# Kernel optimization log

Hardware: AMD Instinct MI355X
Metric: run time of the kernel (lower is better)

The kernel has to match this reference:

```python
import jax, jax.numpy as jnp
import numpy as np

NBITS = 8
QMAX = 2 ** (NBITS - 1) - 1  # 127
EPS_S = 1e-8


def ste_round(x):
    # straight-through estimator round (matches HAWQ ste_round)
    return x + jax.lax.stop_gradient(jnp.round(x) - x)


def quant_act(x):
    # symmetric per-tensor 8-bit fake quantization (QuantAct)
    s = jnp.maximum(jnp.max(jnp.abs(x)) / QMAX, EPS_S)
    xq = jnp.clip(ste_round(x / s), -QMAX - 1, QMAX)
    return xq * s, s


def quant_weight_per_channel(w, axis=0):
    # symmetric per-output-channel 8-bit fake quantization (weights)
    red = tuple(i for i in range(w.ndim) if i != axis)
    s = jnp.maximum(jnp.max(jnp.abs(w), axis=red, keepdims=True) / QMAX, EPS_S)
    wq = jnp.clip(ste_round(w / s), -QMAX - 1, QMAX)
    return wq * s, s


def setup_inputs() -> dict:
    key = jax.random.key(0)
    ks = jax.random.split(key, 6)
    B, Cin, Cout, H, W = 32, 256, 128, 56, 56
    x = jax.random.normal(ks[0], (B, Cin, H, W), jnp.float32)
    bn_gamma = 1.0 + 0.1 * jax.random.normal(ks[1], (Cin,), jnp.float32)
    bn_beta = 0.1 * jax.random.normal(ks[2], (Cin,), jnp.float32)
    bn_mean = 0.1 * jax.random.normal(ks[3], (Cin,), jnp.float32)
    bn_var = jax.random.uniform(ks[4], (Cin,), jnp.float32, minval=0.5, maxval=1.5)
    conv_w = jax.random.normal(ks[5], (Cout, Cin), jnp.float32) * (1.0 / np.sqrt(Cin))
    return {"x": x, "bn_gamma": bn_gamma, "bn_beta": bn_beta,
            "bn_mean": bn_mean, "bn_var": bn_var, "conv_w": conv_w}


def reference(x, bn_gamma, bn_beta, bn_mean, bn_var, conv_w):
    bn_eps = 1e-5
    # --- QuantAct on incoming activations ---
    x, act_s = quant_act(x)
    # --- QuantBn: fold BN into per-channel scale/shift, quantize folded weight ---
    w_fold = bn_gamma * jax.lax.rsqrt(bn_var + bn_eps)        # [Cin]
    b_fold = bn_beta - bn_mean * w_fold                       # [Cin]
    wq, bn_s = quant_weight_per_channel(w_fold, axis=0)
    x = x * wq[None, :, None, None] + b_fold[None, :, None, None]
    # --- QuantAct1: requantize post-BN output (act_s * bn_s threaded) ---
    x, act_s = quant_act(x)
    # --- ReLU ---
    x = jax.nn.relu(x)
    # --- QuantConv2d: 1x1 conv, per-output-channel quantized weight ---
    cwq, conv_s = quant_weight_per_channel(conv_w, axis=0)    # [Cout, Cin]
    x = jnp.einsum('bchw,oc->bohw', x, cwq)                   # [B, Cout, H, W]
    # --- QuantAct2: requantize post-conv output ---
    x, act_s = quant_act(x)
    # --- QuantAveragePool2d(2,2): pool in integer domain, rescale back ---
    B, C, H, W = x.shape
    x_int = x / act_s
    pooled = x_int.reshape(B, C, H // 2, 2, W // 2, 2).mean(axis=(3, 5))
    x = pooled * act_s
    # --- QuantAct3 ---
    x, act_s = quant_act(x)
    return x, act_s
```

## Files before the change

kernel.cpp:

```cpp
#include <hip/hip_runtime.h>
#include <math.h>

#define QMAXF 127.0f
#define EPSF  1e-8f
#define CIN   256
#define COUT  128
#define HW    3136
#define W_    56
#define NPOOL 3211264
#define POOL_BLOCKS 1792

typedef unsigned short u16;
typedef unsigned int   u32;
typedef __attribute__((ext_vector_type(8))) short s16x8;
typedef __attribute__((ext_vector_type(4))) float f32x4;

#define WQ_OFF   8
#define BF_OFF   264
#define EMAX_OFF 520
#define EMIN_OFF 776
#define CS_OFF   1032
#define CSS2_OFF 1160
#define CWB_OFF  1288
#define LUT_OFF  17672
#define Y_OFF    50440

__device__ __forceinline__ float qclip(float v) {
    return fminf(fmaxf(v, -128.0f), 127.0f);
}
__device__ __forceinline__ u16 bf16bits(float f) {
    return (u16)(__float_as_uint(f) >> 16);
}
__device__ __forceinline__ u32 encf(float f) {
    u32 u = __float_as_uint(f);
    return (u & 0x80000000u) ? ~u : (u | 0x80000000u);
}
__device__ __forceinline__ float decf(u32 k) {
    return __uint_as_float((k & 0x80000000u) ? (k ^ 0x80000000u) : ~k);
}

__device__ __forceinline__ void block_max_atomic(float v, float* red, u32* dst) {
    #pragma unroll
    for (int off = 32; off > 0; off >>= 1) v = fmaxf(v, __shfl_xor(v, off));
    const int lane = threadIdx.x & 63, wid = threadIdx.x >> 6;
    if (lane == 0) red[wid] = v;
    __syncthreads();
    if (threadIdx.x == 0) {
        const int nw = blockDim.x >> 6;
        float m = red[0];
        for (int i = 1; i < nw; ++i) m = fmaxf(m, red[i]);
        atomicMax(dst, __float_as_uint(m));
    }
}

__global__ void k0w(const float* __restrict__ cw, float* __restrict__ ws) {
    const int t = threadIdx.x;
    if (blockIdx.x == COUT) {
        ((u32*)ws)[EMAX_OFF + t] = 0u;
        ((u32*)ws)[EMIN_OFF + t] = 0xFFFFFFFFu;
        if (t < 2) ((u32*)ws)[2 + t] = 0u;
        return;
    }
    __shared__ float red[4];
    const int o = blockIdx.x;
    const float wv = cw[o * CIN + t];
    float v = fabsf(wv);
    #pragma unroll
    for (int off = 32; off > 0; off >>= 1) v = fmaxf(v, __shfl_xor(v, off));
    if ((t & 63) == 0) red[t >> 6] = v;
    __syncthreads();
    const float mx = fmaxf(fmaxf(red[0], red[1]), fmaxf(red[2], red[3]));
    const float s = fmaxf(mx / QMAXF, EPSF);
    const float q = qclip(rintf(wv / s));
    ((u16*)(ws + CWB_OFF))[o * CIN + t] = bf16bits(q);
    if (t == 0) ws[CS_OFF + o] = s;
}

__global__ void k1_minmax(const float* __restrict__ x, float* __restrict__ ws) {
    __shared__ float red[8];
    const int row = blockIdx.x;
    const float4* xr = (const float4*)(x + (size_t)row * HW);
    float mx = -3.402823466e38f, mn = 3.402823466e38f;
    for (int i = threadIdx.x; i < HW / 4; i += 256) {
        const float4 v = xr[i];
        mx = fmaxf(mx, fmaxf(fmaxf(v.x, v.y), fmaxf(v.z, v.w)));
        mn = fminf(mn, fminf(fminf(v.x, v.y), fminf(v.z, v.w)));
    }
    #pragma unroll
    for (int off = 32; off > 0; off >>= 1) {
        mx = fmaxf(mx, __shfl_xor(mx, off));
        mn = fminf(mn, __shfl_xor(mn, off));
    }
    if ((threadIdx.x & 63) == 0) {
        red[threadIdx.x >> 6] = mx;
        red[4 + (threadIdx.x >> 6)] = mn;
    }
    __syncthreads();
    if (threadIdx.x == 0) {
        mx = fmaxf(fmaxf(red[0], red[1]), fmaxf(red[2], red[3]));
        mn = fminf(fminf(red[4], red[5]), fminf(red[6], red[7]));
        const int c = row & (CIN - 1);
        atomicMax((u32*)ws + EMAX_OFF + c, encf(mx));
        atomicMin((u32*)ws + EMIN_OFF + c, encf(mn));
    }
}

__global__ void k0b(const float* __restrict__ g, const float* __restrict__ be,
                    const float* __restrict__ mnp, const float* __restrict__ vr,
                    float* __restrict__ ws) {
    __shared__ float red[4];
    __shared__ float s1sh;
    const int t = threadIdx.x;
    const float cmax = decf(((u32*)ws)[EMAX_OFF + t]);
    const float cmin = decf(((u32*)ws)[EMIN_OFF + t]);
    float v = fmaxf(fabsf(cmax), fabsf(cmin));
    #pragma unroll
    for (int off = 32; off > 0; off >>= 1) v = fmaxf(v, __shfl_xor(v, off));
    if ((t & 63) == 0) red[t >> 6] = v;
    __syncthreads();
    if (t == 0) {
        const float m1 = fmaxf(fmaxf(red[0], red[1]), fmaxf(red[2], red[3]));
        ws[0] = m1;
        s1sh = fmaxf(m1 / QMAXF, EPSF);
    }
    __syncthreads();
    const float s1 = s1sh;
    const float wf = g[t] / sqrtf(vr[t] + 1e-5f);
    const float bf = be[t] - mnp[t] * wf;
    const float sw = fmaxf(fabsf(wf) / QMAXF, EPSF);
    const float q  = qclip(rintf(wf / sw));
    const float wqd = __fmul_rn(q, sw);
    ws[WQ_OFF + t] = wqd;
    ws[BF_OFF + t] = bf;
    const float q1h = qclip(rintf(cmax / s1));
    const float q1l = qclip(rintf(cmin / s1));
    const float xh = __fadd_rn(__fmul_rn(__fmul_rn(q1h, s1), wqd), bf);
    const float xl = __fadd_rn(__fmul_rn(__fmul_rn(q1l, s1), wqd), bf);
    float m2 = fmaxf(fabsf(xh), fabsf(xl));
    __syncthreads();
    #pragma unroll
    for (int off = 32; off > 0; off >>= 1) m2 = fmaxf(m2, __shfl_xor(m2, off));
    if ((t & 63) == 0) red[t >> 6] = m2;
    __syncthreads();
    if (t == 0) ws[1] = fmaxf(fmaxf(red[0], red[1]), fmaxf(red[2], red[3]));
}

__global__ void k0L(float* __restrict__ ws) {
    const int c = blockIdx.x;
    const int t = threadIdx.x;
    const float s1 = fmaxf(ws[0] / QMAXF, EPSF);
    const float s2 = fmaxf(ws[1] / QMAXF, EPSF);
    const float wqd = ws[WQ_OFF + c];
    const float bf  = ws[BF_OFF + c];
    const float q1f = (float)(t - 127);
    const float xd  = __fmul_rn(q1f, s1);
    const float x2  = __fadd_rn(__fmul_rn(xd, wqd), bf);
    const float q2  = qclip(rintf(x2 / s2));
    const float a   = fmaxf(q2, 0.0f);
    ((u16*)(ws + LUT_OFF))[(c << 8) + t] = bf16bits(a);
    if (c == 0 && t < COUT)
        ws[CSS2_OFF + t] = __fmul_rn(s2, ws[CS_OFF + t]);
}

__global__ __launch_bounds__(256) void k3_mfma(const float* __restrict__ x,
                                               float* __restrict__ ws) {
    __shared__ __align__(16) u16 Xs[32 * 256];
    __shared__ float Css2s[COUT];
    __shared__ float red[4];

    const int t   = threadIdx.x;
    const int b   = blockIdx.x / 98;
    const int hw0 = (blockIdx.x % 98) * 32;
    const int l   = t & 63, w = t >> 6;
    const int wc  = w * 32;

    const float s1 = fmaxf(ws[0] / QMAXF, EPSF);
    const double rinv1 = 1.0 / (double)s1;
    const u16* lut = (const u16*)(ws + LUT_OFF);
    const u16* cwb = (const u16*)(ws + CWB_OFF);

    if (t < COUT) Css2s[t] = ws[CSS2_OFF + t];

    const int p  = t & 31;
    const int kh = t >> 5;
    const float* xb = x + (size_t)b * CIN * HW + hw0 + p;
    const int sw8 = ((kh + p + (p >> 3)) & 7) * 8;

    #pragma unroll
    for (int g = 0; g < 4; ++g) {
        float xv[8];
        #pragma unroll
        for (int j = 0; j < 8; ++j)
            xv[j] = xb[(g * 64 + kh * 8 + j) * HW];
        u32 pk[4];
        #pragma unroll
        for (int jj = 0; jj < 4; ++jj) {
            const int c0 = g * 64 + kh * 8 + 2 * jj;
            const u32 qa = (u32)((int)rintf((float)((double)xv[2 * jj]     * rinv1)) + 127);
            const u32 qb = (u32)((int)rintf((float)((double)xv[2 * jj + 1] * rinv1)) + 127);
            const u32 lo = lut[(c0 << 8) + qa];
            const u32 hi = lut[((c0 + 1) << 8) + qb];
            pk[jj] = lo | (hi << 16);
        }
        uint4 v; v.x = pk[0]; v.y = pk[1]; v.z = pk[2]; v.w = pk[3];
        *(uint4*)&Xs[p * 256 + g * 64 + sw8] = v;
    }
    __syncthreads();

    f32x4 acc[2][2];
    #pragma unroll
    for (int m = 0; m < 2; ++m)
        #pragma unroll
        for (int n = 0; n < 2; ++n) acc[m][n] = (f32x4)0.0f;

    const int lm = l & 15, lh = l >> 4;
    const u16* wbase0 = cwb + (wc + lm) * CIN + lh * 8;
    const u16* wbase1 = cwb + (wc + 16 + lm) * CIN + lh * 8;

    #pragma unroll
    for (int it = 0; it < 4; ++it) {
        #pragma unroll
        for (int ks = 0; ks < 2; ++ks) {
            const int ch = ks * 4 + lh;
            const int ko = it * 64 + ks * 32;
            s16x8 xf[2], wfr[2];
            #pragma unroll
            for (int n = 0; n < 2; ++n) {
                const int pp = n * 16 + lm;
                xf[n] = *(const s16x8*)&Xs[pp * 256 + it * 64 +
                                           (((ch + pp + (pp >> 3)) & 7) * 8)];
            }
            wfr[0] = *(const s16x8*)(wbase0 + ko);
            wfr[1] = *(const s16x8*)(wbase1 + ko);
            #pragma unroll
            for (int m = 0; m < 2; ++m)
                #pragma unroll
                for (int n = 0; n < 2; ++n)
                    acc[m][n] = __builtin_amdgcn_mfma_f32_16x16x32_bf16(
                                    wfr[m], xf[n], acc[m][n], 0, 0, 0);
        }
    }

    float mloc = 0.0f;
    #pragma unroll
    for (int m = 0; m < 2; ++m) {
        #pragma unroll
        for (int n = 0; n < 2; ++n) {
            const int pix = hw0 + n * 16 + lm;
            #pragma unroll
            for (int r = 0; r < 4; ++r) {
                const int o = wc + m * 16 + lh * 4 + r;
                const float val = __fmul_rn(acc[m][n][r], Css2s[o]);
                ws[Y_OFF + ((size_t)(b * COUT + o)) * HW + pix] = val;
                mloc = fmaxf(mloc, fabsf(val));
            }
        }
    }
    block_max_atomic(mloc, red, (u32*)ws + 2);
}

__global__ void k4_pool(float* __restrict__ ws, float* __restrict__ out) {
    __shared__ float red[4];
    const float s3 = fmaxf(ws[2] / QMAXF, EPSF);
    float mloc = 0.0f;
    const int nq2 = NPOOL / 2;
    for (int pp = blockIdx.x * 256 + threadIdx.x; pp < nq2;
         pp += POOL_BLOCKS * 256) {
        const int j2  = pp % 14;
        const int tmp = pp / 14;
        const int i   = tmp % 28;
        const int bo  = tmp / 28;
        const float* yb = ws + Y_OFF + (size_t)bo * HW + (2 * i) * W_ + 4 * j2;
        const float4 r0 = *(const float4*)yb;
        const float4 r1 = *(const float4*)(yb + W_);
        const float q00 = qclip(rintf(r0.x / s3)), q01 = qclip(rintf(r0.y / s3));
        const float q02 = qclip(rintf(r0.z / s3)), q03 = qclip(rintf(r0.w / s3));
        const float q10 = qclip(rintf(r1.x / s3)), q11 = qclip(rintf(r1.y / s3));
        const float q12 = qclip(rintf(r1.z / s3)), q13 = qclip(rintf(r1.w / s3));
        const float p0 = __fmul_rn(__fmul_rn((q00 + q01) + (q10 + q11), 0.25f), s3);
        const float p1 = __fmul_rn(__fmul_rn((q02 + q03) + (q12 + q13), 0.25f), s3);
        float2 pv; pv.x = p0; pv.y = p1;
        *(float2*)(out + (size_t)bo * 784 + i * 28 + 2 * j2) = pv;
        mloc = fmaxf(mloc, fmaxf(fabsf(p0), fabsf(p1)));
    }
    block_max_atomic(mloc, red, (u32*)ws + 3);
}

__global__ void k5_final(float* __restrict__ out, const float* __restrict__ ws) {
    const float s4 = fmaxf(ws[3] / QMAXF, EPSF);
    const int n4 = NPOOL / 4;
    for (int i = blockIdx.x * 256 + threadIdx.x; i < n4; i += 3136 * 256) {
        float4 v = *(float4*)(out + 4 * (size_t)i);
        v.x = __fmul_rn(qclip(rintf(v.x / s4)), s4);
        v.y = __fmul_rn(qclip(rintf(v.y / s4)), s4);
        v.z = __fmul_rn(qclip(rintf(v.z / s4)), s4);
        v.w = __fmul_rn(qclip(rintf(v.w / s4)), s4);
        *(float4*)(out + 4 * (size_t)i) = v;
    }
    if (blockIdx.x == 0 && threadIdx.x == 0) out[NPOOL] = s4;
}

extern "C" void kernel_launch(void* const* d_in, const int* in_sizes, int n_in,
                              void* d_out, int out_size, void* d_ws, size_t ws_size,
                              hipStream_t stream) {
    const float* x     = (const float*)d_in[0];
    const float* gamma = (const float*)d_in[1];
    const float* beta  = (const float*)d_in[2];
    const float* mean  = (const float*)d_in[3];
    const float* var   = (const float*)d_in[4];
    const float* cw    = (const float*)d_in[5];
    float* out = (float*)d_out;
    float* ws  = (float*)d_ws;

    hipLaunchKernelGGL(k0w, dim3(COUT + 1), dim3(256), 0, stream, cw, ws);
    hipLaunchKernelGGL(k1_minmax, dim3(32 * CIN), dim3(256), 0, stream, x, ws);
    hipLaunchKernelGGL(k0b, dim3(1), dim3(256), 0, stream, gamma, beta, mean, var, ws);
    hipLaunchKernelGGL(k0L, dim3(256), dim3(256), 0, stream, ws);
    hipLaunchKernelGGL(k3_mfma, dim3(3136), dim3(256), 0, stream, x, ws);
    hipLaunchKernelGGL(k4_pool, dim3(POOL_BLOCKS), dim3(256), 0, stream, ws, out);
    hipLaunchKernelGGL(k5_final, dim3(3136), dim3(256), 0, stream, out, ws);
}
```

Baseline: 121.6 us.

## Replace per-channel requant LUT with inline arithmetic and drop LUT kernel

Removes the k0L kernel that built a 256x256 bf16 lookup table for the BN+requant+ReLU mapping. k3_mfma now computes that mapping inline from per-channel scale/shift staged in shared memory, and the CSS2 computation moves into k0b. All 32 x loads are hoisted before the arithmetic so more loads are in flight, and launch bounds ask for 6 blocks per CU. This saves a launch and the scattered global LUT gathers, at the cost of extra double-precision divides and ALU work plus higher register pressure from the 32-float buffer.

```diff
diff --git a/kernel.cpp b/kernel.cpp
--- a/kernel.cpp
+++ b/kernel.cpp
@@ -22,7 +22,6 @@
 #define CS_OFF   1032
 #define CSS2_OFF 1160
 #define CWB_OFF  1288
-#define LUT_OFF  17672
 #define Y_OFF    50440
 
 __device__ __forceinline__ float qclip(float v) {
@@ -109,7 +108,7 @@
                     const float* __restrict__ mnp, const float* __restrict__ vr,
                     float* __restrict__ ws) {
     __shared__ float red[4];
-    __shared__ float s1sh;
+    __shared__ float s1sh, s2sh;
     const int t = threadIdx.x;
     const float cmax = decf(((u32*)ws)[EMAX_OFF + t]);
     const float cmin = decf(((u32*)ws)[EMIN_OFF + t]);
@@ -142,29 +141,19 @@
     for (int off = 32; off > 0; off >>= 1) m2 = fmaxf(m2, __shfl_xor(m2, off));
     if ((t & 63) == 0) red[t >> 6] = m2;
     __syncthreads();
-    if (t == 0) ws[1] = fmaxf(fmaxf(red[0], red[1]), fmaxf(red[2], red[3]));
-}
-
-__global__ void k0L(float* __restrict__ ws) {
-    const int c = blockIdx.x;
-    const int t = threadIdx.x;
-    const float s1 = fmaxf(ws[0] / QMAXF, EPSF);
-    const float s2 = fmaxf(ws[1] / QMAXF, EPSF);
-    const float wqd = ws[WQ_OFF + c];
-    const float bf  = ws[BF_OFF + c];
-    const float q1f = (float)(t - 127);
-    const float xd  = __fmul_rn(q1f, s1);
-    const float x2  = __fadd_rn(__fmul_rn(xd, wqd), bf);
-    const float q2  = qclip(rintf(x2 / s2));
-    const float a   = fmaxf(q2, 0.0f);
-    ((u16*)(ws + LUT_OFF))[(c << 8) + t] = bf16bits(a);
-    if (c == 0 && t < COUT)
-        ws[CSS2_OFF + t] = __fmul_rn(s2, ws[CS_OFF + t]);
-}
-
-__global__ __launch_bounds__(256) void k3_mfma(const float* __restrict__ x,
-                                               float* __restrict__ ws) {
+    if (t == 0) {
+        const float m2f = fmaxf(fmaxf(red[0], red[1]), fmaxf(red[2], red[3]));
+        ws[1] = m2f;
+        s2sh = fmaxf(m2f / QMAXF, EPSF);
+    }
+    __syncthreads();
+    if (t < COUT) ws[CSS2_OFF + t] = __fmul_rn(s2sh, ws[CS_OFF + t]);
+}
+
+__global__ __launch_bounds__(256, 6) void k3_mfma(const float* __restrict__ x,
+                                                  float* __restrict__ ws) {
     __shared__ __align__(16) u16 Xs[32 * 256];
+    __shared__ float2 wqbfs[CIN];
     __shared__ float Css2s[COUT];
     __shared__ float red[4];
 
@@ -175,32 +164,47 @@
     const int wc  = w * 32;
 
     const float s1 = fmaxf(ws[0] / QMAXF, EPSF);
+    const float s2 = fmaxf(ws[1] / QMAXF, EPSF);
     const double rinv1 = 1.0 / (double)s1;
-    const u16* lut = (const u16*)(ws + LUT_OFF);
+    const double rinv2 = 1.0 / (double)s2;
     const u16* cwb = (const u16*)(ws + CWB_OFF);
-
-    if (t < COUT) Css2s[t] = ws[CSS2_OFF + t];
 
     const int p  = t & 31;
     const int kh = t >> 5;
     const float* xb = x + (size_t)b * CIN * HW + hw0 + p;
     const int sw8 = ((kh + p + (p >> 3)) & 7) * 8;
 
+    float xv[32];
+    #pragma unroll
+    for (int g = 0; g < 4; ++g)
+        #pragma unroll
+        for (int j = 0; j < 8; ++j)
+            xv[g * 8 + j] = xb[(g * 64 + kh * 8 + j) * HW];
+
+    float2 wb0; wb0.x = ws[WQ_OFF + t]; wb0.y = ws[BF_OFF + t];
+    wqbfs[t] = wb0;
+    if (t < COUT) Css2s[t] = ws[CSS2_OFF + t];
+    __syncthreads();
+
     #pragma unroll
     for (int g = 0; g < 4; ++g) {
-        float xv[8];
-        #pragma unroll
-        for (int j = 0; j < 8; ++j)
-            xv[j] = xb[(g * 64 + kh * 8 + j) * HW];
         u32 pk[4];
         #pragma unroll
         for (int jj = 0; jj < 4; ++jj) {
-            const int c0 = g * 64 + kh * 8 + 2 * jj;
-            const u32 qa = (u32)((int)rintf((float)((double)xv[2 * jj]     * rinv1)) + 127);
-            const u32 qb = (u32)((int)rintf((float)((double)xv[2 * jj + 1] * rinv1)) + 127);
-            const u32 lo = lut[(c0 << 8) + qa];
-            const u32 hi = lut[((c0 + 1) << 8) + qb];
-            pk[jj] = lo | (hi << 16);
+            float a2[2];
+            #pragma unroll
+            for (int u = 0; u < 2; ++u) {
+                const int k = g * 8 + 2 * jj + u;
+                const int c = g * 64 + kh * 8 + 2 * jj + u;
+                const float2 wb = wqbfs[c];
+                const float q1 = rintf((float)((double)xv[k] * rinv1));
+                const float xd = __fmul_rn(q1, s1);
+                const float x2 = __fadd_rn(__fmul_rn(xd, wb.x), wb.y);
+                const float q2 = rintf((float)((double)x2 * rinv2));
+                a2[u] = fminf(fmaxf(q2, 0.0f), 127.0f);
+            }
+            pk[jj] = (__float_as_uint(a2[0]) >> 16) |
+                     (__float_as_uint(a2[1]) & 0xFFFF0000u);
         }
         uint4 v; v.x = pk[0]; v.y = pk[1]; v.z = pk[2]; v.w = pk[3];
         *(uint4*)&Xs[p * 256 + g * 64 + sw8] = v;
@@ -315,7 +319,6 @@
     hipLaunchKernelGGL(k0w, dim3(COUT + 1), dim3(256), 0, stream, cw, ws);
     hipLaunchKernelGGL(k1_minmax, dim3(32 * CIN), dim3(256), 0, stream, x, ws);
     hipLaunchKernelGGL(k0b, dim3(1), dim3(256), 0, stream, gamma, beta, mean, var, ws);
-    hipLaunchKernelGGL(k0L, dim3(256), dim3(256), 0, stream, ws);
     hipLaunchKernelGGL(k3_mfma, dim3(3136), dim3(256), 0, stream, x, ws);
     hipLaunchKernelGGL(k4_pool, dim3(POOL_BLOCKS), dim3(256), 0, stream, ws, out);
     hipLaunchKernelGGL(k5_final, dim3(3136), dim3(256), 0, stream, out, ws);
```

Measured after the change: 211.0 us. 1.74x slower.

## Process four tiles per block with double-buffered LDS and prefetched float4 loads

Applied to the files above, without the earlier changes.

The MFMA conv kernel now handles four 32-pixel tiles per block (784 blocks instead of 3136). It double-buffers the LDS activation tile and prefetches the next tile's inputs into registers while the current tile's MFMAs run. Global loads are widened to float4 along pixels, and there is one block-max atomic per four tiles. The aim is to overlap global-load latency with compute and to cut per-block overhead. The cost is more registers and fewer blocks, which could lower occupancy.

```diff
diff --git a/kernel.cpp b/kernel.cpp
--- a/kernel.cpp
+++ b/kernel.cpp
@@ -164,95 +164,130 @@
 
 __global__ __launch_bounds__(256) void k3_mfma(const float* __restrict__ x,
                                                float* __restrict__ ws) {
-    __shared__ __align__(16) u16 Xs[32 * 256];
+    __shared__ __align__(16) u16 Xs[2][32 * 256];
     __shared__ float Css2s[COUT];
     __shared__ float red[4];
 
-    const int t   = threadIdx.x;
-    const int b   = blockIdx.x / 98;
-    const int hw0 = (blockIdx.x % 98) * 32;
-    const int l   = t & 63, w = t >> 6;
-    const int wc  = w * 32;
+    const int t  = threadIdx.x;
+    const int l  = t & 63, w = t >> 6;
+    const int wc = w * 32;
+    const int lm = l & 15, lh = l >> 4;
 
     const float s1 = fmaxf(ws[0] / QMAXF, EPSF);
     const double rinv1 = 1.0 / (double)s1;
     const u16* lut = (const u16*)(ws + LUT_OFF);
     const u16* cwb = (const u16*)(ws + CWB_OFF);
-
     if (t < COUT) Css2s[t] = ws[CSS2_OFF + t];
 
-    const int p  = t & 31;
-    const int kh = t >> 5;
-    const float* xb = x + (size_t)b * CIN * HW + hw0 + p;
-    const int sw8 = ((kh + p + (p >> 3)) & 7) * 8;
-
-    #pragma unroll
-    for (int g = 0; g < 4; ++g) {
-        float xv[8];
+    const int pg  = (t & 7) * 4;
+    const int cb  = (t >> 3) * 8;
+    const int qg  = cb >> 6;
+    const int chl = (cb >> 3) & 7;
+
+    const u16* wb0 = cwb + (wc + lm) * CIN + lh * 8;
+    const u16* wb1 = cwb + (wc + 16 + lm) * CIN + lh * 8;
+
+    const int tid0 = blockIdx.x * 4;
+
+    float4 xv[8];
+    {
+        const int b = tid0 / 98, hw0 = (tid0 % 98) * 32;
+        const float* xb = x + ((size_t)b * CIN + cb) * HW + hw0 + pg;
         #pragma unroll
         for (int j = 0; j < 8; ++j)
-            xv[j] = xb[(g * 64 + kh * 8 + j) * HW];
-        u32 pk[4];
+            xv[j] = *(const float4*)(xb + j * HW);
+    }
+
+    float mloc = 0.0f;
+
+    #pragma unroll
+    for (int tt = 0; tt < 4; ++tt) {
+        const int tid = tid0 + tt;
+        const int b = tid / 98, hw0 = (tid % 98) * 32;
+
+        {
+            u32 pk[4][4];
+            #pragma unroll
+            for (int u = 0; u < 4; ++u)
+                #pragma unroll
+                for (int q = 0; q < 4; ++q) pk[u][q] = 0u;
+            #pragma unroll
+            for (int j = 0; j < 8; ++j) {
+                const u16* row = lut + ((cb + j) << 8);
+                const float vv[4] = {xv[j].x, xv[j].y, xv[j].z, xv[j].w};
+                #pragma unroll
+                for (int u = 0; u < 4; ++u) {
+                    const int qi = (int)rintf((float)((double)vv[u] * rinv1)) + 127;
+                    pk[u][j >> 1] |= ((u32)row[qi]) << ((j & 1) * 16);
+                }
+            }
+            u16* Xb = Xs[tt & 1];
+            #pragma unroll
+            for (int u = 0; u < 4; ++u) {
+                const int p = pg + u;
+                uint4 v; v.x = pk[u][0]; v.y = pk[u][1]; v.z = pk[u][2]; v.w = pk[u][3];
+                *(uint4*)&Xb[p * 256 + qg * 64 + (((chl + p + (p >> 3)) & 7) * 8)] = v;
+            }
+        }
+
+        if (tt < 3) {
+            const int tid1 = tid + 1;
+            const int b1 = tid1 / 98, hw01 = (tid1 % 98) * 32;
+            const float* xb = x + ((size_t)b1 * CIN + cb) * HW + hw01 + pg;
+            #pragma unroll
+            for (int j = 0; j < 8; ++j)
+                xv[j] = *(const float4*)(xb + j * HW);
+            #pragma unroll
+            for (int j = 0; j < 8; ++j)
+                asm volatile("" : "+v"(xv[j].x), "+v"(xv[j].y),
+                                  "+v"(xv[j].z), "+v"(xv[j].w));
+        }
+
+        __syncthreads();
+
+        f32x4 acc[2][2];
         #pragma unroll
-        for (int jj = 0; jj < 4; ++jj) {
-            const int c0 = g * 64 + kh * 8 + 2 * jj;
-            const u32 qa = (u32)((int)rintf((float)((double)xv[2 * jj]     * rinv1)) + 127);
-            const u32 qb = (u32)((int)rintf((float)((double)xv[2 * jj + 1] * rinv1)) + 127);
-            const u32 lo = lut[(c0 << 8) + qa];
-            const u32 hi = lut[((c0 + 1) << 8) + qb];
-            pk[jj] = lo | (hi << 16);
+        for (int m = 0; m < 2; ++m)
+            #pragma unroll
+            for (int n = 0; n < 2; ++n) acc[m][n] = (f32x4)0.0f;
+
+        const u16* Xb = Xs[tt & 1];
+        #pragma unroll
+        for (int it = 0; it < 4; ++it) {
+            #pragma unroll
+            for (int ks = 0; ks < 2; ++ks) {
+                const int ch = ks * 4 + lh;
+                const int ko = it * 64 + ks * 32;
+                s16x8 xf[2], wfr[2];
+                #pragma unroll
+                for (int n = 0; n < 2; ++n) {
+                    const int pp = n * 16 + lm;
+                    xf[n] = *(const s16x8*)&Xb[pp * 256 + it * 64 +
+                                               (((ch + pp + (pp >> 3)) & 7) * 8)];
+                }
+                wfr[0] = *(const s16x8*)(wb0 + ko);
+                wfr[1] = *(const s16x8*)(wb1 + ko);
+                #pragma unroll
+                for (int m = 0; m < 2; ++m)
+                    #pragma unroll
+                    for (int n = 0; n < 2; ++n)
+                        acc[m][n] = __builtin_amdgcn_mfma_f32_16x16x32_bf16(
+                                        wfr[m], xf[n], acc[m][n], 0, 0, 0);
+            }
         }
-        uint4 v; v.x = pk[0]; v.y = pk[1]; v.z = pk[2]; v.w = pk[3];
-        *(uint4*)&Xs[p * 256 + g * 64 + sw8] = v;
-    }
-    __syncthreads();
-
-    f32x4 acc[2][2];
-    #pragma unroll
-    for (int m = 0; m < 2; ++m)
+
         #pragma unroll
-        for (int n = 0; n < 2; ++n) acc[m][n] = (f32x4)0.0f;
-
-    const int lm = l & 15, lh = l >> 4;
-    const u16* wbase0 = cwb + (wc + lm) * CIN + lh * 8;
-    const u16* wbase1 = cwb + (wc + 16 + lm) * CIN + lh * 8;
-
-    #pragma unroll
-    for (int it = 0; it < 4; ++it) {
-        #pragma unroll
-        for (int ks = 0; ks < 2; ++ks) {
-            const int ch = ks * 4 + lh;
-            const int ko = it * 64 + ks * 32;
-            s16x8 xf[2], wfr[2];
+        for (int m = 0; m < 2; ++m) {
             #pragma unroll
             for (int n = 0; n < 2; ++n) {
-                const int pp = n * 16 + lm;
-                xf[n] = *(const s16x8*)&Xs[pp * 256 + it * 64 +
-                                           (((ch + pp + (pp >> 3)) & 7) * 8)];
-            }
-            wfr[0] = *(const s16x8*)(wbase0 + ko);
-            wfr[1] = *(const s16x8*)(wbase1 + ko);
-            #pragma unroll
-            for (int m = 0; m < 2; ++m)
-                #pragma unroll
-                for (int n = 0; n < 2; ++n)
-                    acc[m][n] = __builtin_amdgcn_mfma_f32_16x16x32_bf16(
-                                    wfr[m], xf[n], acc[m][n], 0, 0, 0);
-        }
-    }
-
-    float mloc = 0.0f;
-    #pragma unroll
-    for (int m = 0; m < 2; ++m) {
-        #pragma unroll
-        for (int n = 0; n < 2; ++n) {
-            const int pix = hw0 + n * 16 + lm;
-            #pragma unroll
-            for (int r = 0; r < 4; ++r) {
-                const int o = wc + m * 16 + lh * 4 + r;
-                const float val = __fmul_rn(acc[m][n][r], Css2s[o]);
-                ws[Y_OFF + ((size_t)(b * COUT + o)) * HW + pix] = val;
-                mloc = fmaxf(mloc, fabsf(val));
+                const int pix = hw0 + n * 16 + lm;
+                #pragma unroll
+                for (int r = 0; r < 4; ++r) {
+                    const int o = wc + m * 16 + lh * 4 + r;
+                    const float val = __fmul_rn(acc[m][n][r], Css2s[o]);
+                    ws[Y_OFF + ((size_t)(b * COUT + o)) * HW + pix] = val;
+                    mloc = fmaxf(mloc, fabsf(val));
+                }
             }
         }
     }
@@ -316,7 +351,7 @@
     hipLaunchKernelGGL(k1_minmax, dim3(32 * CIN), dim3(256), 0, stream, x, ws);
     hipLaunchKernelGGL(k0b, dim3(1), dim3(256), 0, stream, gamma, beta, mean, var, ws);
     hipLaunchKernelGGL(k0L, dim3(256), dim3(256), 0, stream, ws);
-    hipLaunchKernelGGL(k3_mfma, dim3(3136), dim3(256), 0, stream, x, ws);
+    hipLaunchKernelGGL(k3_mfma, dim3(784), dim3(256), 0, stream, x, ws);
     hipLaunchKernelGGL(k4_pool, dim3(POOL_BLOCKS), dim3(256), 0, stream, ws, out);
     hipLaunchKernelGGL(k5_final, dim3(3136), dim3(256), 0, stream, out, ws);
 }
```

After: 134.1 us. +10.2%, slower.
